# Performance work log

Hardware: AMD Instinct MI355X
Metric: run time of the kernel (lower is better)

The kernel has to match this reference:

```python
import jax, jax.numpy as jnp
import numpy as np

B, C, H, W = 2, 64, 128, 128
HEADS, DH = 8, 32
DN = ('NCHW', 'OIHW', 'NCHW')


def _conv(x, w, pad):
    return jax.lax.conv_general_dilated(x, w, (1, 1), [(pad, pad), (pad, pad)], dimension_numbers=DN)


def _rconv3(x, w):
    # Conv3x3 module: ReflectionPad2d(1) then 3x3 VALID conv, no bias
    xp = jnp.pad(x, ((0, 0), (0, 0), (1, 1), (1, 1)), mode='reflect')
    return jax.lax.conv_general_dilated(xp, w, (1, 1), 'VALID', dimension_numbers=DN)


def _prelu(x, a):
    return jnp.where(x > 0, x, a * x)


def _l2n(x):
    # F.normalize(p=2, dim=-1), eps=1e-12
    return x / jnp.maximum(jnp.linalg.norm(x, axis=-1, keepdims=True), 1e-12)


def _ln(y, g, b):
    mu = y.mean(-1, keepdims=True)
    v = ((y - mu) ** 2).mean(-1, keepdims=True)
    return (y - mu) / jnp.sqrt(v + 1e-5) * g + b


def _qco(x, w1, sw, sb, t1w, t1b, t2w, t2b):
    # QCO_C with level_num == C
    b, Cc = x.shape[0], x.shape[1]
    L = Cc
    x1 = _rconv3(x, w1)
    x_ave = _conv(jnp.mean(x1, (2, 3), keepdims=True), sw, 0) + sb[None, :, None, None]  # [b,C,1,1]
    xq = x_ave.reshape(b, Cc)
    mn = xq.min(-1, keepdims=True)
    mx = xq.max(-1, keepdims=True)
    qs = jnp.arange(L, dtype=x.dtype)
    ql = (2.0 * qs + 1.0) / (2.0 * L) * (mx - mn) + mn  # [b,L]
    inter = (ql[:, 1] - ql[:, 0])[:, None, None]  # [b,1,1]
    quant = 1.0 - jnp.abs(ql[:, None, :] - xq[:, :, None])  # [b,C,L]
    quant = quant * (quant > 1.0 - inter)
    sta = quant.sum(1)  # [b,L]
    sta = sta / sta.sum(-1, keepdims=True)
    out = jnp.concatenate([sta[:, :, None, None], x_ave], axis=1)  # [b,2C,1,1]
    out = jax.nn.relu(_conv(out, t1w, 0) + t1b[None, :, None, None])
    out = jax.nn.relu(_conv(out, t2w, 0) + t2b[None, :, None, None])
    return out  # [b,C,1,1]


def _attention(x, w_down, w_mid, w_up, wq_l, wk_m, wv_m, wq_h, rescale,
               w_proj_l, b_proj_l, w_proj_h, b_proj_h,
               qco_w1, qco_sca_w, qco_sca_b, qco_t1_w, qco_t1_b, qco_t2_w, qco_t2_b,
               rsp_w1, rsp_prelu, rsp_w2, c31_w1, c31_prelu, c31_w2, c31_w3):
    b, Cc, Hh, Ww = x.shape
    n = Hh * Ww
    # QKV conv projections (Conv2d, zero pad 1, no bias)
    xCL = jnp.moveaxis(_conv(x, w_down, 1), 1, -1)  # [b,h,w,C]
    xCM = jnp.moveaxis(_conv(x, w_mid, 1), 1, -1)   # [b,h,w,2C]
    xCH = jnp.moveaxis(_conv(x, w_up, 1), 1, -1)    # [b,h,w,3C]
    xL = xCL.reshape(b, n, Cc)
    xM = xCM.reshape(b, n, 2 * Cc)
    xH = xCH.reshape(b, n, 3 * Cc)

    def to_heads(t, d):  # [b,n,heads*d] -> [b,heads,d,n]
        return t.reshape(b, n, HEADS, d).transpose(0, 2, 3, 1)

    q_l = _l2n(to_heads(xL @ wq_l.T, DH))            # [b,heads,DH,n]
    k_m = _l2n(to_heads(xM @ wk_m.T, 2 * DH))        # [b,heads,2DH,n]
    v_m = to_heads(xM @ wv_m.T, 2 * DH)              # [b,heads,2DH,n]
    q_h = _l2n(to_heads(xH @ wq_h.T, 3 * DH))        # [b,heads,3DH,n]

    attn_l = jax.nn.softmax(jnp.einsum('bhdn,bhen->bhde', q_l, k_m) * rescale, axis=-1)  # [b,heads,DH,2DH]
    attn_h = jax.nn.softmax(jnp.einsum('bhdn,bhen->bhde', q_h, k_m) * rescale, axis=-1)  # [b,heads,3DH,2DH]

    x_l = jnp.einsum('bhde,bhen->bhdn', attn_l, v_m).transpose(0, 3, 1, 2).reshape(b, n, HEADS * DH)
    x_h = jnp.einsum('bhde,bhen->bhdn', attn_h, v_m).transpose(0, 3, 1, 2).reshape(b, n, HEADS * 3 * DH)
    # NOTE: torch code does .view(b, c, h, w) on [b, n, c] output -> raw memory reinterpretation,
    # which is exactly jnp.reshape here (faithful to the original, including this quirk).
    out_cl = (x_l @ w_proj_l.T + b_proj_l).reshape(b, Cc, Hh, Ww)
    out_ch = (x_h @ w_proj_h.T + b_proj_h).reshape(b, 3 * Cc, Hh, Ww)

    Hcat = jnp.concatenate([out_cl, out_ch], axis=1)  # [b,4C,h,w]
    H_out = _rconv3(_prelu(_rconv3(Hcat, rsp_w1), rsp_prelu), rsp_w2)  # ReshapeBlock -> [b,C,h,w]
    att_before = _qco(jnp.moveaxis(xCL, -1, 1), qco_w1, qco_sca_w, qco_sca_b,
                      qco_t1_w, qco_t1_b, qco_t2_w, qco_t2_b)  # [b,C,1,1]
    t = _prelu(_rconv3(H_out, c31_w1), c31_prelu)
    H_add = _conv(_rconv3(t, c31_w2), c31_w3, 0)  # Conv3_1
    return H_add + H_out * att_before


def _ff_block(z, g, bb, w1, b1, w2, b2):
    # PreNorm(LayerNorm over channel) + FeedForward(Linear, LeakyReLU(0.01), Linear)
    y = jnp.moveaxis(z, 1, -1)
    y = _ln(y, g, bb)
    y = y @ w1.T + b1
    y = jnp.where(y > 0, y, 0.01 * y)
    y = y @ w2.T + b2
    return jnp.moveaxis(y, -1, 1)


def _forward(x, w_down, w_mid, w_up, wq_l, wk_m, wv_m, wq_h, rescale,
             w_proj_l, b_proj_l, w_proj_h, b_proj_h,
             qco_w1, qco_sca_w, qco_sca_b, qco_t1_w, qco_t1_b, qco_t2_w, qco_t2_b,
             rsp_w1, rsp_prelu, rsp_w2, c31_w1, c31_prelu, c31_w2, c31_w3,
             ln1_g, ln1_b, ff1_w1, ff1_b1, ff1_w2, ff1_b2,
             ln2_g, ln2_b, ff2_w1, ff2_b1, ff2_w2, ff2_b2):
    out1 = _attention(x, w_down, w_mid, w_up, wq_l, wk_m, wv_m, wq_h, rescale,
                      w_proj_l, b_proj_l, w_proj_h, b_proj_h,
                      qco_w1, qco_sca_w, qco_sca_b, qco_t1_w, qco_t1_b, qco_t2_w, qco_t2_b,
                      rsp_w1, rsp_prelu, rsp_w2, c31_w1, c31_prelu, c31_w2, c31_w3) + x
    out2 = _ff_block(out1, ln1_g, ln1_b, ff1_w1, ff1_b1, ff1_w2, ff1_b2) + out1
    out3 = _ff_block(out2, ln2_g, ln2_b, ff2_w1, ff2_b1, ff2_w2, ff2_b2) + out1
    return out3


def setup_inputs() -> dict:
    keys = iter(jax.random.split(jax.random.key(0), 48))

    def rn(shape, s=0.05):
        return (jax.random.normal(next(keys), shape, jnp.float32) * s)

    d = {
        'x': rn((B, C, H, W), 1.0),
        'w_down': rn((C, C, 3, 3)), 'w_mid': rn((2 * C, C, 3, 3)), 'w_up': rn((3 * C, C, 3, 3)),
        'wq_l': rn((HEADS * DH, C)), 'wk_m': rn((2 * HEADS * DH, 2 * C)),
        'wv_m': rn((2 * HEADS * DH, 2 * C)), 'wq_h': rn((3 * HEADS * DH, 3 * C)),
        'rescale': jnp.ones((HEADS, 1, 1), jnp.float32),
        'w_proj_l': rn((C, HEADS * DH)), 'b_proj_l': rn((C,)),
        'w_proj_h': rn((3 * C, 3 * HEADS * DH)), 'b_proj_h': rn((3 * C,)),
        'qco_w1': rn((C, C, 3, 3)), 'qco_sca_w': rn((C, C, 1, 1)), 'qco_sca_b': rn((C,)),
        'qco_t1_w': rn((C, 2 * C, 1, 1)), 'qco_t1_b': rn((C,)),
        'qco_t2_w': rn((C, C, 1, 1)), 'qco_t2_b': rn((C,)),
        'rsp_w1': rn((C, 4 * C, 3, 3)), 'rsp_prelu': jnp.array(0.25, jnp.float32), 'rsp_w2': rn((C, C, 3, 3)),
        'c31_w1': rn((C, C, 3, 3)), 'c31_prelu': jnp.array(0.25, jnp.float32),
        'c31_w2': rn((C, C, 3, 3)), 'c31_w3': rn((C, C, 1, 1)),
        'ln1_g': jnp.ones((C,), jnp.float32), 'ln1_b': jnp.zeros((C,), jnp.float32),
        'ff1_w1': rn((C, C)), 'ff1_b1': rn((C,)), 'ff1_w2': rn((C, C)), 'ff1_b2': rn((C,)),
        'ln2_g': jnp.ones((C,), jnp.float32), 'ln2_b': jnp.zeros((C,), jnp.float32),
        'ff2_w1': rn((C, C)), 'ff2_b1': rn((C,)), 'ff2_w2': rn((C, C)), 'ff2_b2': rn((C,)),
    }
    return d


def reference(x, w_down, w_mid, w_up, wq_l, wk_m, wv_m, wq_h, rescale,
              w_proj_l, b_proj_l, w_proj_h, b_proj_h,
              qco_w1, qco_sca_w, qco_sca_b, qco_t1_w, qco_t1_b, qco_t2_w, qco_t2_b,
              rsp_w1, rsp_prelu, rsp_w2, c31_w1, c31_prelu, c31_w2, c31_w3,
              ln1_g, ln1_b, ff1_w1, ff1_b1, ff1_w2, ff1_b2,
              ln2_g, ln2_b, ff2_w1, ff2_b1, ff2_w2, ff2_b2):
    return _forward(x, w_down, w_mid, w_up, wq_l, wk_m, wv_m, wq_h, rescale,
                    w_proj_l, b_proj_l, w_proj_h, b_proj_h,
                    qco_w1, qco_sca_w, qco_sca_b, qco_t1_w, qco_t1_b, qco_t2_w, qco_t2_b,
                    rsp_w1, rsp_prelu, rsp_w2, c31_w1, c31_prelu, c31_w2, c31_w3,
                    ln1_g, ln1_b, ff1_w1, ff1_b1, ff1_w2, ff1_b2,
                    ln2_g, ln2_b, ff2_w1, ff2_b1, ff2_w2, ff2_b2)
```

## Files before the change

### kernel.cpp

```cpp
#include <hip/hip_runtime.h>
#include <hip/hip_bf16.h>
#include <stdint.h>

typedef __hip_bfloat16 bf16;
typedef __attribute__((ext_vector_type(8))) __bf16 bf8v;
typedef __attribute__((ext_vector_type(8))) short short8;
typedef __attribute__((ext_vector_type(4))) short short4v;
typedef __attribute__((ext_vector_type(4))) float f32x4;
#define DEVINL __device__ __forceinline__
#define MFMA16(a,b,c) __builtin_amdgcn_mfma_f32_16x16x32_bf16((a),(b),(c),0,0,0)

DEVINL short f2bs(float f) { bf16 h = __float2bfloat16(f); return *reinterpret_cast<short*>(&h); }
DEVINL float bs2f(short s) { bf16 h = *reinterpret_cast<bf16*>(&s); return __bfloat162float(h); }


static const size_t OFF_ZBF   = 0;
static const size_t OFF_WTQ   = 29360128;
static const size_t OFF_WTR1  = 29802496;
static const size_t OFF_WTR2  = 30097408;
static const size_t OFF_WTC1  = 30171136;
static const size_t OFF_WTF   = 30244864;
static const size_t OFF_W1T   = 30318592;
static const size_t OFF_SCAWT = 30466048;
static const size_t OFF_T1WT  = 30482432;
static const size_t OFF_T2WT  = 30515200;
static const size_t OFF_GB    = 31645696;
static const size_t OFF_WQLB  = 32235520;
static const size_t OFF_WKMB  = 32268288;
static const size_t OFF_WQHB  = 32399360;
static const size_t OFF_T1    = 41082880;
static const size_t OFF_UL    = 41345024;
static const size_t OFF_UK    = 41476096;
static const size_t OFF_T1H   = 42000384;
static const size_t OFF_UH    = 42786816;
static const size_t OFF_NORMS = 43966464;
static const size_t OFF_ATTL  = 43978752;
static const size_t OFF_ATTH  = 44109824;
static const size_t OFF_WEL   = 44503040;
static const size_t OFF_WEH   = 44765184;
static const size_t OFF_ACATB = 45813760;
static const size_t OFF_TSUM  = 45944832;
static const size_t OFF_ATTB  = 45949440;
static const size_t OFF_HCATB = 45949952;
static const size_t OFF_MIDB  = 62727168;
static const size_t OFF_HOUTB = 66921472;
static const size_t OFF_WFFB  = 71115776;
static const size_t OFF_GPART = 79504384;
static const size_t OFF_HCATT = 79504384;
static const size_t OFF_XT    = 98378752;
static const size_t WS_BYTES  = 102573056;

__global__ __launch_bounds__(256) void k_prep_all(
    const float* __restrict__ wd, const float* __restrict__ wm,
    const float* __restrict__ wu, const float* __restrict__ rw1,
    const float* __restrict__ rw2, const float* __restrict__ cw1,
    const float* __restrict__ wql, const float* __restrict__ wkm,
    const float* __restrict__ wqh,
    const float* __restrict__ c31w3, const float* __restrict__ c31w2,
    const float* __restrict__ qw1, const float* __restrict__ qscaw,
    const float* __restrict__ qt1w, const float* __restrict__ qt2w,
    const float* __restrict__ f11, const float* __restrict__ f12,
    const float* __restrict__ f21, const float* __restrict__ f22,
    const float* __restrict__ x,
    bf16* __restrict__ wtq, bf16* __restrict__ wtr1,
    bf16* __restrict__ wtr2, bf16* __restrict__ wtc1,
    bf16* __restrict__ wqlb, bf16* __restrict__ wkmb,
    bf16* __restrict__ wqhb, bf16* __restrict__ wtf,
    float* __restrict__ w1t, float* __restrict__ scawt,
    float* __restrict__ t1wt, float* __restrict__ t2wt,
    bf16* __restrict__ wffb, short* __restrict__ xt) {
  __shared__ short sT[64][72];
  const int t = threadIdx.x;
  if (blockIdx.x >= 3040) {
    const int j = blockIdx.x - 3040;
    const int b = j >> 8, p0 = (j & 255) * 64;
    for (int i = t; i < 1024; i += 256) {
      int c = i >> 4, p4 = (i & 15) * 4;
      float4 g = *(const float4*)&x[(((size_t)(b * 64 + c)) << 14) + p0 + p4];
      sT[p4 + 0][c] = f2bs(g.x);
      sT[p4 + 1][c] = f2bs(g.y);
      sT[p4 + 2][c] = f2bs(g.z);
      sT[p4 + 3][c] = f2bs(g.w);
    }
    __syncthreads();
    for (int i = t; i < 512; i += 256) {
      int p = i >> 3, co = (i & 7) * 8;
      *(short8*)&xt[((((size_t)b << 14) + p0 + p)) * 64 + co] = *(short8*)&sT[p][co];
    }
    return;
  }
  int i = blockIdx.x * 256 + t;
  if (i < 221184) {
    int tap = i / 24576, r = i % 24576, oc = r >> 6, ic = r & 63;
    float v;
    if (oc < 64)       v = wd[(oc * 64 + ic) * 9 + tap];
    else if (oc < 192) v = wm[((oc - 64) * 64 + ic) * 9 + tap];
    else               v = wu[((oc - 192) * 64 + ic) * 9 + tap];
    wtq[i] = __float2bfloat16(v);
  } else if (i < 368640) {
    int j = i - 221184;
    int tap = j / 16384, r = j % 16384, oc = r >> 8, ic = r & 255;
    wtr1[j] = __float2bfloat16(rw1[(oc * 256 + ic) * 9 + tap]);
  } else if (i < 405504) {
    int j = i - 368640;
    int tap = j / 4096, r = j % 4096, oc = r >> 6, ic = r & 63;
    wtr2[j] = __float2bfloat16(rw2[(oc * 64 + ic) * 9 + tap]);
  } else if (i < 442368) {
    int j = i - 405504;
    int tap = j / 4096, r = j % 4096, oc = r >> 6, ic = r & 63;
    wtc1[j] = __float2bfloat16(cw1[(oc * 64 + ic) * 9 + tap]);
  } else if (i < 458752) {
    int j = i - 442368; wqlb[j] = __float2bfloat16(wql[j]);
  } else if (i < 524288) {
    int j = i - 458752; wkmb[j] = __float2bfloat16(wkm[j]);
  } else if (i < 671744) {
    int j = i - 524288; wqhb[j] = __float2bfloat16(wqh[j]);
  } else if (i < 708608) {
    int j = i - 671744;
    int tap = j / 4096, r = j % 4096, o = r >> 6, ic = r & 63;
    float s = 0.f;
    for (int m = 0; m < 64; m++)
      s = fmaf(c31w3[o * 64 + m], c31w2[(m * 64 + ic) * 9 + tap], s);
    wtf[j] = __float2bfloat16(s);
  } else if (i < 745472) {
    int o = i - 708608;
    int c = o & 63, rest = o >> 6, jj = rest / 9, tap = rest % 9;
    w1t[o] = qw1[(c * 64 + jj) * 9 + tap];
  } else if (i < 749568) {
    int o = i - 745472;
    int c = o & 63, jj = o >> 6;
    scawt[o] = qscaw[c * 64 + jj];
  } else if (i < 757760) {
    int o = i - 749568;
    int c = o & 63, jj = o >> 6;
    t1wt[o] = qt1w[c * 128 + jj];
  } else if (i < 761856) {
    int o = i - 757760;
    int c = o & 63, jj = o >> 6;
    t2wt[o] = qt2w[c * 64 + jj];
  } else if (i < 778240) {
    int j = i - 761856;
    int stage = j >> 12, r = j & 4095;
    const float* src = (stage == 0) ? f11 : (stage == 1) ? f12 : (stage == 2) ? f21 : f22;
    wffb[j] = __float2bfloat16(src[r]);
  }
}

__global__ __launch_bounds__(256) void k_transph(const short* __restrict__ hc,
                                                 short* __restrict__ ht) {
  __shared__ short sT[64][72];
  const int t = threadIdx.x, b = blockIdx.z, p0 = blockIdx.x * 64, c0 = blockIdx.y * 64;
  for (int i = t; i < 512; i += 256) {
    int c = i >> 3, qo = (i & 7) * 8;
    short8 v = *(const short8*)&hc[(((size_t)(b * 256 + c0 + c)) << 14) + p0 + qo];
#pragma unroll
    for (int u = 0; u < 8; u++) sT[qo + u][c] = v[u];
  }
  __syncthreads();
  for (int i = t; i < 512; i += 256) {
    int q = i >> 3, co = (i & 7) * 8;
    *(short8*)&ht[((size_t)(b * 16384 + p0 + q)) * 256 + c0 + co] = *(short8*)&sT[q][co];
  }
}

__global__ __launch_bounds__(256) void k_convq(
    const short* __restrict__ xt, const short* __restrict__ wtq,
    bf16* __restrict__ zbf)
{
  __shared__ short sX[3][130][72];
  const int t = threadIdx.x, lane = t & 63, wv = t >> 6;
  const int y = blockIdx.x, ocg = blockIdx.y, b = blockIdx.z;

  for (int i = t; i < 3120; i += 256) {
    int ko = i & 7, c2 = i >> 3, col = c2 % 130, row = c2 / 130;
    int gy = y + row - 1, gx = col - 1;
    short8 vv;
    if ((gy >= 0) & (gy < 128) & (gx >= 0) & (gx < 128)) {
      vv = *(const short8*)&xt[((size_t)b * 1048576 + (size_t)((gy << 7) + gx) * 64) + ko * 8];
    } else {
#pragma unroll
      for (int u = 0; u < 8; u++) vv[u] = 0;
    }
    *(short8*)&sX[row][col][ko * 8] = vv;
  }
  __syncthreads();

  const f32x4 zero = {0.f, 0.f, 0.f, 0.f};
  f32x4 acc[3][8];
#pragma unroll
  for (int m = 0; m < 3; m++)
// ... 113 lines not shown
  __shared__ float sv[64][68];
  __shared__ short sy[64][72];
  __shared__ float spar[8][64];
  const int t = threadIdx.x, lane = t & 63, wv = t >> 6;
  const int y = blockIdx.x, x0 = blockIdx.y * 64, b = blockIdx.z;

  if (t < 64) {
    spar[0][t] = g1[t]; spar[1][t] = be1[t]; spar[2][t] = b11[t]; spar[3][t] = b12[t];
    spar[4][t] = g2[t]; spar[5][t] = be2[t]; spar[6][t] = b21[t]; spar[7][t] = b22[t];
  }
  for (int i = t; i < 1584; i += 256) {
    int ko = i & 7, c2 = i >> 3, col = c2 % 66, row = c2 / 66;
    int gy = y + row - 1, gx = x0 + col - 1;
    gy = gy < 0 ? 1 : (gy > 127 ? 126 : gy);
    gx = gx < 0 ? 1 : (gx > 127 ? 126 : gx);
    *(short8*)&sX[row][col][ko * 8] =
        *(const short8*)&in[(size_t)b * 1048576 + (size_t)((gy << 7) + gx) * 64 + ko * 8];
  }
  __syncthreads();

  const f32x4 zero = {0.f, 0.f, 0.f, 0.f};
  {
    f32x4 cacc[4] = {zero, zero, zero, zero};
#pragma unroll
    for (int tap = 0; tap < 9; tap++) {
      const int ky = tap / 3, kx = tap % 3;
#pragma unroll
      for (int kk = 0; kk < 2; kk++) {
        const int kb = kk * 32 + (lane >> 4) * 8;
        bf8v afr = *(const bf8v*)&Wt[(size_t)(tap * 64 + wv * 16 + (lane & 15)) * 64 + kb];
#pragma unroll
        for (int n = 0; n < 4; n++) {
          bf8v bfr = *(const bf8v*)&sX[ky][n * 16 + (lane & 15) + kx][kb];
          cacc[n] = MFMA16(afr, bfr, cacc[n]);
        }
      }
    }
    const int oc0 = wv * 16 + ((lane >> 4) << 2);
    float4 av = *(const float4*)&attb[b * 64 + oc0];
#pragma unroll
    for (int n = 0; n < 4; n++) {
      const int pxl = n * 16 + (lane & 15);
      const int gpx = (y << 7) + x0 + pxl;
      short4v hv = *(const short4v*)&houtpm[((size_t)(b * 16384 + gpx)) * 64 + oc0];
#pragma unroll
      for (int r = 0; r < 4; r++)
        sv[pxl][oc0 + r] = cacc[n][r] + bs2f(hv[r]) * (&av.x)[r] +
                           x_nchw[(((size_t)(b * 64 + oc0 + r)) << 14) + gpx];
    }
  }
  __syncthreads();

  const int chq = ((lane >> 4) << 2);
  const int pxl = wv * 16 + (lane & 15);
  float4 vv[4];
#pragma unroll
  for (int m = 0; m < 4; m++) vv[m] = *(const float4*)&sv[pxl][m * 16 + chq];

  f32x4 facc[4];

#define LN_F(SRCV, GI, BI)                                                      \
  {                                                                             \
    float s1 = 0.f, s2 = 0.f;                                                   \
    _Pragma("unroll")                                                           \
    for (int m = 0; m < 4; m++)                                                 \
      _Pragma("unroll")                                                         \
      for (int r = 0; r < 4; r++) {                                             \
        float vx = (&SRCV[m].x)[r];                                             \
        s1 += vx; s2 += vx * vx;                                                \
      }                                                                         \
    s1 += __shfl_xor(s1, 16); s1 += __shfl_xor(s1, 32);                         \
    s2 += __shfl_xor(s2, 16); s2 += __shfl_xor(s2, 32);                         \
    float mu = s1 * (1.f / 64.f);                                               \
    float var = fmaxf(s2 * (1.f / 64.f) - mu * mu, 0.f);                        \
    float rstd = 1.f / sqrtf(var + 1e-5f);                                      \
    _Pragma("unroll")                                                           \
    for (int m = 0; m < 4; m++) {                                               \
      short4v ss;                                                               \
      _Pragma("unroll")                                                         \
      for (int r = 0; r < 4; r++) {                                             \
        int ch = m * 16 + chq + r;                                              \
        ss[r] = f2bs(((&SRCV[m].x)[r] - mu) * rstd * spar[GI][ch] + spar[BI][ch]); \
      }                                                                         \
      *(short4v*)&sy[pxl][m * 16 + chq] = ss;                                   \
    }                                                                           \
  }

#define MM_F(SIDX)                                                              \
  {                                                                             \
    _Pragma("unroll")                                                           \
    for (int m = 0; m < 4; m++) facc[m] = zero;                                 \
    _Pragma("unroll")                                                           \
    for (int kk = 0; kk < 2; kk++) {                                            \
      const int kb = kk * 32 + (lane >> 4) * 8;                                 \
      bf8v bfr = *(const bf8v*)&sy[wv * 16 + (lane & 15)][kb];                  \
      _Pragma("unroll")                                                         \
      for (int m = 0; m < 4; m++) {                                             \
        bf8v afr = *(const bf8v*)&wffb[(size_t)(SIDX) * 4096 +                  \
                                       (m * 16 + (lane & 15)) * 64 + kb];       \
        facc[m] = MFMA16(afr, bfr, facc[m]);                                    \
      }                                                                         \
    }                                                                           \
  }

  LN_F(vv, 0, 1);
  MM_F(0);
#pragma unroll
  for (int m = 0; m < 4; m++) {
    short4v ss;
#pragma unroll
    for (int r = 0; r < 4; r++) {
      float h = facc[m][r] + spar[2][m * 16 + chq + r];
      h = h > 0.f ? h : 0.01f * h;
      ss[r] = f2bs(h);
    }
    *(short4v*)&sy[pxl][m * 16 + chq] = ss;
  }
  MM_F(1);
  float4 o2v[4];
#pragma unroll
  for (int m = 0; m < 4; m++)
#pragma unroll
    for (int r = 0; r < 4; r++)
      (&o2v[m].x)[r] = facc[m][r] + spar[3][m * 16 + chq + r] + (&vv[m].x)[r];
  LN_F(o2v, 4, 5);
  MM_F(2);
#pragma unroll
  for (int m = 0; m < 4; m++) {
    short4v ss;
#pragma unroll
    for (int r = 0; r < 4; r++) {
      float h = facc[m][r] + spar[6][m * 16 + chq + r];
      h = h > 0.f ? h : 0.01f * h;
      ss[r] = f2bs(h);
    }
    *(short4v*)&sy[pxl][m * 16 + chq] = ss;
  }
  MM_F(3);
  const int gpx = (y << 7) + x0 + pxl;
#pragma unroll
  for (int m = 0; m < 4; m++)
#pragma unroll
    for (int r = 0; r < 4; r++) {
      const int ch = m * 16 + chq + r;
      outp[(((size_t)(b * 64 + ch)) << 14) + gpx] =
          facc[m][r] + spar[7][ch] + (&vv[m].x)[r];
    }
#undef LN_F
#undef MM_F
}

__global__ __launch_bounds__(256) void k_gramm(const short* __restrict__ Z,
                                               float* __restrict__ Gp) {
  int rem = blockIdx.x, ti = 0;
  while (rem >= 6 - ti) { rem -= 6 - ti; ti++; }
  const int tj = ti + rem;
  const int kc = blockIdx.y, b = blockIdx.z;
  __shared__ short sA[64][72];
  __shared__ short sB[64][72];
  const int t = threadIdx.x, lane = t & 63, wv = t >> 6;
  const int wo = wv & 1, wp = wv >> 1;
  const f32x4 zero = {0.f, 0.f, 0.f, 0.f};
  f32x4 acc[2][2];
#pragma unroll
  for (int m = 0; m < 2; m++)
#pragma unroll
    for (int n = 0; n < 2; n++) acc[m][n] = zero;
  const size_t zb = (size_t)b * 6291456;
  const int k0 = kc * 1024;
  for (int ks = 0; ks < 1024; ks += 64) {
    __syncthreads();
    for (int i = t; i < 512; i += 256) {
      int r = i >> 3, ko = i & 7;
      *(short8*)&sA[r][ko * 8] =
          *(const short8*)&Z[zb + ((size_t)(ti * 64 + r) << 14) + k0 + ks + ko * 8];
      *(short8*)&sB[r][ko * 8] =
          *(const short8*)&Z[zb + ((size_t)(tj * 64 + r) << 14) + k0 + ks + ko * 8];
    }
    __syncthreads();
#pragma unroll
    for (int kk = 0; kk < 2; kk++) {
      const int kb = kk * 32 + (lane >> 4) * 8;
      bf8v bfr[2];
#pragma unroll
      for (int n = 0; n < 2; n++)
        bfr[n] = *(const bf8v*)&sB[wp * 32 + n * 16 + (lane & 15)][kb];
#pragma unroll
      for (int m = 0; m < 2; m++) {
        bf8v afr = *(const bf8v*)&sA[wo * 32 + m * 16 + (lane & 15)][kb];
#pragma unroll
        for (int n = 0; n < 2; n++)
          acc[m][n] = MFMA16(afr, bfr[n], acc[m][n]);
      }
    }
  }
  float* gp = Gp + ((size_t)(kc * 2 + b)) * 147456;
#pragma unroll
  for (int m = 0; m < 2; m++)
#pragma unroll
    for (int n = 0; n < 2; n++)
#pragma unroll
      for (int r = 0; r < 4; r++) {
        const int row = ti * 64 + wo * 32 + m * 16 + ((lane >> 4) << 2) + r;
        const int col = tj * 64 + wp * 32 + n * 16 + (lane & 15);
        float v = acc[m][n][r];
        gp[(size_t)row * 384 + col] = v;
        if (ti != tj) gp[(size_t)col * 384 + row] = v;
      }
}

__global__ __launch_bounds__(256) void k_gt(const float* __restrict__ Gp,
                                            bf16* __restrict__ Gb,
                                            const bf16* __restrict__ Z,
                                            float* __restrict__ Tsum) {
  __shared__ float sc[16];
  __shared__ float red[4][9];
  const int t = threadIdx.x;
  if (blockIdx.x < 1152) {
    int i = blockIdx.x * 256 + t;
    if (i >= 294912) return;
    int b = i / 147456, e = i % 147456;
    float s = 0.f;
#pragma unroll
    for (int c = 0; c < 16; c++) s += Gp[(size_t)(c * 2 + b) * 147456 + e];
    Gb[(size_t)b * 147456 + e] = __float2bfloat16(s);
    return;
  }
  const int bid = blockIdx.x - 1152;
  const int c = bid & 63, b = bid >> 6;
  const bf16* src = Z + (((size_t)(b * 384 + c)) << 14);
  float a9[9] = {};
  for (int i = t; i < 2048; i += 256) {
    int y = i >> 4, x0 = (i & 15) * 8;
    short8 v8 = *(const short8*)&src[(y << 7) + x0];
    float vs[8], s8 = 0.f;
#pragma unroll
    for (int u = 0; u < 8; u++) { vs[u] = bs2f(v8[u]); s8 += vs[u]; }
    a9[0] += s8;
    int ri = (y == 0) ? 0 : (y == 1) ? 1 : (y == 126) ? 2 : (y == 127) ? 3 : -1;
    if (ri >= 0) a9[1 + ri] += s8;
    if (x0 == 0)   { a9[5] += vs[0]; a9[6] += vs[1]; }
    if (x0 == 120) { a9[7] += vs[6]; a9[8] += vs[7]; }
    if (ri >= 0) {
      if (x0 == 0)   { sc[ri * 4 + 0] = vs[0]; sc[ri * 4 + 1] = vs[1]; }
      if (x0 == 120) { sc[ri * 4 + 2] = vs[6]; sc[ri * 4 + 3] = vs[7]; }
    }
  }
#pragma unroll
  for (int q = 0; q < 9; q++)
#pragma unroll
    for (int o = 32; o; o >>= 1) a9[q] += __shfl_xor(a9[q], o);
  const int w = t >> 6;
  if ((t & 63) == 0)
#pragma unroll
    for (int q = 0; q < 9; q++) red[w][q] = a9[q];
  __syncthreads();
  if (t == 0) {
    float s9[9];
#pragma unroll
    for (int q = 0; q < 9; q++) s9[q] = red[0][q] + red[1][q] + red[2][q] + red[3][q];
    const float T = s9[0];
    float R[4] = {s9[1], s9[2], s9[3], s9[4]};
    const float C0 = s9[5], C1 = s9[6], C126 = s9[7], C127 = s9[8];
    float rs[4][3];
#pragma unroll
    for (int ri = 0; ri < 4; ri++) {
      rs[ri][0] = R[ri] - sc[ri * 4 + 3] + sc[ri * 4 + 1];
      rs[ri][1] = R[ri];
      rs[ri][2] = R[ri] - sc[ri * 4 + 0] + sc[ri * 4 + 2];
    }
    float A3[3] = {T - C127 + C1, T, T - C0 + C126};
#pragma unroll
    for (int dx = 0; dx < 3; dx++) {
      Tsum[bid * 9 + 0 * 3 + dx] = A3[dx] - rs[3][dx] + rs[1][dx];
      Tsum[bid * 9 + 1 * 3 + dx] = A3[dx];
      Tsum[bid * 9 + 2 * 3 + dx] = A3[dx] - rs[0][dx] + rs[2][dx];
    }
  }
}

struct MJobs5 {
  const short* A[5];
  float* C[5];
  int lda[5], K[5], r0[5], c0[5], ldc[5];
  long sC[5];
  int nx[5], b0[6];
};

__global__ __launch_bounds__(256) void k_mgemm5(MJobs5 J, const short* __restrict__ Gb) {
  const int bx = blockIdx.x, z = blockIdx.y;
  int j = 0;
  while (bx >= J.b0[j + 1]) j++;
  const int local = bx - J.b0[j];
  const int xn = local % J.nx[j], ym = local / J.nx[j];
  const int t = threadIdx.x, lane = t & 63, wv = t >> 6;
  const short* Gp = Gb + (size_t)z * 147456;
  const short* Ap = J.A[j];
  const int K = J.K[j], lda = J.lda[j];
  const int m0 = ym * 64 + wv * 16, n0 = xn * 64;
  const int gc0 = J.c0[j] + n0, r0 = J.r0[j];
  const f32x4 zero = {0.f, 0.f, 0.f, 0.f};
  f32x4 acc[4] = {zero, zero, zero, zero};
  for (int kk = 0; kk < K; kk += 32) {
    const int kb = kk + (lane >> 4) * 8;
    bf8v afr = *(const bf8v*)&Ap[(size_t)(m0 + (lane & 15)) * lda + kb];
#pragma unroll
    for (int n = 0; n < 4; n++) {
      bf8v bfr = *(const bf8v*)&Gp[(size_t)(gc0 + n * 16 + (lane & 15)) * 384 + r0 + kb];
      acc[n] = MFMA16(afr, bfr, acc[n]);
    }
  }
  float* Cp = J.C[j] + (size_t)z * J.sC[j];
  const int mq = m0 + ((lane >> 4) << 2);
#pragma unroll
  for (int n = 0; n < 4; n++) {
    const int nc = n0 + n * 16 + (lane & 15);
#pragma unroll
    for (int r = 0; r < 4; r++)
      Cp[(size_t)(mq + r) * J.ldc[j] + nc] = acc[n][r];
  }
}

__global__ __launch_bounds__(256) void k_pixm(
    const short* __restrict__ Z, const short* __restrict__ Acatb,
    const float* __restrict__ bl, const float* __restrict__ bh,
    bf16* __restrict__ hcat)
{
  const int p0 = blockIdx.x * 64, ocg = blockIdx.y, b = blockIdx.z;
  __shared__ short sA[64][136];
  __shared__ short sB[64][136];
  const int t = threadIdx.x, lane = t & 63, wv = t >> 6;
  for (int i = t; i < 1024; i += 256) {
    int oc = i >> 4, ko = i & 15;
    *(short8*)&sA[oc][ko * 8] =
        *(const short8*)&Acatb[((size_t)(b * 256 + ocg * 64 + oc)) * 128 + ko * 8];
  }
  for (int i = t; i < 1024; i += 256) {
    int px = i & 63, ko = i >> 6;
    short8 vv;
#pragma unroll
    for (int u = 0; u < 8; u++)
      vv[u] = Z[((size_t)(b * 384 + 64 + ko * 8 + u) << 14) + p0 + px];
    *(short8*)&sB[px][ko * 8] = vv;
  }
  __syncthreads();
  const f32x4 zero = {0.f, 0.f, 0.f, 0.f};
  f32x4 acc[4] = {zero, zero, zero, zero};
#pragma unroll
  for (int kk = 0; kk < 4; kk++) {
    const int kb = kk * 32 + (lane >> 4) * 8;
    bf8v afr = *(const bf8v*)&sA[wv * 16 + (lane & 15)][kb];
#pragma unroll
    for (int n = 0; n < 4; n++) {
      bf8v bfr = *(const bf8v*)&sB[n * 16 + (lane & 15)][kb];
      acc[n] = MFMA16(afr, bfr, acc[n]);
    }
  }
  const size_t hbase = (size_t)b * 4194304;
#pragma unroll
  for (int n = 0; n < 4; n++) {
    const int px = p0 + n * 16 + (lane & 15);
#pragma unroll
    for (int r = 0; r < 4; r++) {
      const int oc = ocg * 64 + wv * 16 + ((lane >> 4) << 2) + r;
      float v = acc[n][r] + (oc < 64 ? bl[oc] : bh[oc - 64]);
      size_t addr = (oc < 64) ? hbase + (size_t)px * 64 + oc
                              : hbase + 1048576 + (size_t)px * 192 + (oc - 64);
      hcat[addr] = __float2bfloat16(v);
    }
  }
}

struct Jobs2 {
  const float* A[2]; const float* B[2];
  int K[2]; int lda[2];
  long sB[2];
  int nx[2]; int b0[3]; int co[2];
};

__global__ __launch_bounds__(256) void k_sgemm2b(Jobs2 J, bf16* __restrict__ Cb) {
  __shared__ float sa[16][17];
  __shared__ float sb[16][17];
  const int bx = blockIdx.x, z = blockIdx.y;
  int j = (bx >= J.b0[1]) ? 1 : 0;
  const int local = bx - J.b0[j];
  const int x = local % J.nx[j], y = local / J.nx[j];
  const int tx = threadIdx.x & 15, ty = threadIdx.x >> 4;
  const float* Ap = J.A[j];
  const float* Bp = J.B[j] + (size_t)z * J.sB[j];
  const int K = J.K[j], lda = J.lda[j];
  const int m = y * 16 + ty, n = x * 16 + tx;
  float acc = 0.f;
  for (int k0 = 0; k0 < K; k0 += 16) {
    sa[ty][tx] = Ap[(size_t)m * lda + k0 + tx];
    sb[ty][tx] = Bp[(size_t)(k0 + ty) * 128 + n];
    __syncthreads();
#pragma unroll
    for (int kk = 0; kk < 16; kk++) acc = fmaf(sa[ty][kk], sb[kk][tx], acc);
    __syncthreads();
  }
  Cb[(size_t)z * 32768 + J.co[j] + (size_t)m * 128 + n] = __float2bfloat16(acc);
}

__global__ __launch_bounds__(256) void k_nq(
    const float* __restrict__ UL, const float* __restrict__ UK,
    const float* __restrict__ UH,
    const float* __restrict__ wql, const float* __restrict__ wkm,
    const float* __restrict__ wqh, float* __restrict__ norms,
    const float* __restrict__ Tsum, const float* __restrict__ w1t,
    const float* __restrict__ scawt, const float* __restrict__ scab,
    const float* __restrict__ t1wt, const float* __restrict__ t1b,
    const float* __restrict__ t2wt, const float* __restrict__ t2b,
    float* __restrict__ attb)
{
  __shared__ float sm[64], sxq[64], scat[128], sh1[64];
  const int t = threadIdx.x, lane = t & 63;
  if (blockIdx.x < 768) {
    const int row = blockIdx.x * 4 + (t >> 6);
    const int b = row >= 1536 ? 1 : 0;
    const int r = row - b * 1536;
    const float* u; const float* wv; int K;
    if (r < 256)      { K = 64;  u = UL + (size_t)(b * 256 + r) * 64;          wv = wql + (size_t)r * 64; }
    else if (r < 768) { int e = r - 256; K = 128; u = UK + (size_t)(b * 512 + e) * 128; wv = wkm + (size_t)e * 128; }
    else              { int d = r - 768; K = 192; u = UH + (size_t)(b * 768 + d) * 192; wv = wqh + (size_t)d * 192; }
    float s = 0.f;
    for (int k = lane; k < K; k += 64) s = fmaf(u[k], wv[k], s);
#pragma unroll
    for (int o = 32; o; o >>= 1) s += __shfl_xor(s, o);
    if (lane == 0) norms[b * 1536 + r] = fmaxf(sqrtf(fmaxf(s, 0.f)), 1e-12f);
    return;
  }
  const int b = blockIdx.x - 768, c = t;
  if (t < 64) {
    float acc = 0.f;
    for (int j = 0; j < 64; j++) {
#pragma unroll
      for (int tap = 0; tap < 9; tap++)
        acc = fmaf(w1t[((j * 9 + tap) << 6) + c], Tsum[(b * 64 + j) * 9 + tap], acc);
    }
    sm[c] = acc * (1.f / 16384.f);
  }
  __syncthreads();
  if (t < 64) {
    float xa = scab[c];
    for (int j = 0; j < 64; j++) xa = fmaf(scawt[(j << 6) + c], sm[j], xa);
    sxq[c] = xa;
  }
  __syncthreads();
  if (t < 64) {
    float xa = sxq[c];
    float mn = xa, mx = xa;
#pragma unroll
    for (int o = 32; o; o >>= 1) {
      mn = fminf(mn, __shfl_xor(mn, o));
      mx = fmaxf(mx, __shfl_xor(mx, o));
    }
    float inter = (mx - mn) * (1.f / 64.f);
    float ql = (2.f * c + 1.f) / 128.f * (mx - mn) + mn;
    float sta = 0.f;
    for (int j = 0; j < 64; j++) {
      float q = 1.f - fabsf(ql - sxq[j]);
      sta += (q > 1.f - inter) ? q : 0.f;
    }
    float tot = sta;
#pragma unroll
    for (int o = 32; o; o >>= 1) tot += __shfl_xor(tot, o);
    sta = sta / fmaxf(tot, 1e-30f);
    scat[c] = sta; scat[64 + c] = xa;
  }
  __syncthreads();
  if (t < 64) {
    float h = t1b[c];
    for (int j = 0; j < 128; j++) h = fmaf(t1wt[(j << 6) + c], scat[j], h);
    h = fmaxf(h, 0.f);
    sh1[c] = h;
  }
  __syncthreads();
  if (t < 64) {
    float o2 = t2b[c];
    for (int j = 0; j < 64; j++) o2 = fmaf(t2wt[(j << 6) + c], sh1[j], o2);
    attb[b * 64 + c] = fmaxf(o2, 0.f);
  }
}

__global__ __launch_bounds__(256) void k_attn(
    const float* __restrict__ T1, const float* __restrict__ T1H,
    const float* __restrict__ wkm, const float* __restrict__ norms,
    const float* __restrict__ rescale,
    float* __restrict__ attL, float* __restrict__ attH)
{
  const int h = blockIdx.x, cy = blockIdx.y, b = blockIdx.z;
  const int t = threadIdx.x;
  __shared__ float sK[64 * 129];
  __shared__ float sQ[32 * 129];
  __shared__ float sNk[64];
  const int isL = (cy == 0);
  const int rbase = isL ? 0 : (cy - 1) * 32;
  const float* TQ = isL ? (T1 + (size_t)(b * 256 + h * 32) * 128)
                        : (T1H + (size_t)(b * 768 + h * 96 + rbase) * 128);
  for (int idx = t; idx < 8192; idx += 256) {
    int e = idx >> 7, k = idx & 127;
    sK[e * 129 + k] = wkm[(size_t)(h * 64 + e) * 128 + k];
  }
  for (int idx = t; idx < 4096; idx += 256) {
    int r = idx >> 7, k = idx & 127;
    sQ[r * 129 + k] = TQ[(size_t)r * 128 + k];
  }
  if (t < 64) sNk[t] = norms[b * 1536 + 256 + h * 64 + t];
  __syncthreads();

  const int w = t >> 6, lane = t & 63;
  const float rs = rescale[h];
  for (int r = w; r < 32; r += 4) {
    float s = 0.f;
    for (int k = 0; k < 128; k++) s = fmaf(sQ[r * 129 + k], sK[lane * 129 + k], s);
    float nq = norms[b * 1536 + (isL ? (h * 32 + r) : (768 + h * 96 + rbase + r))];
    float logit = s / (nq * sNk[lane]) * rs;
    float m = logit;
#pragma unroll
    for (int o = 32; o; o >>= 1) m = fmaxf(m, __shfl_xor(m, o));
    float p = __expf(logit - m);
    float den = p;
#pragma unroll
    for (int o = 32; o; o >>= 1) den += __shfl_xor(den, o);
    float av = p / den;
    if (isL) attL[((size_t)(b * 8 + h) * 32 + r) * 64 + lane] = av;
    else     attH[((size_t)(b * 8 + h) * 96 + rbase + r) * 64 + lane] = av;
  }
}

__global__ __launch_bounds__(256) void k_weff(
    const float* __restrict__ attL, const float* __restrict__ attH,
    const float* __restrict__ wvm,
    float* __restrict__ WeL, float* __restrict__ WeH)
{
  const int h = blockIdx.x, br = blockIdx.y, b = blockIdx.z;
  const int M = br ? 96 : 32;
  __shared__ float sAt[96 * 64];
  __shared__ float sV[64 * 132];
  const int t = threadIdx.x;
  const float* asrc = br ? attH + (size_t)(b * 8 + h) * 96 * 64
                         : attL + (size_t)(b * 8 + h) * 32 * 64;
  for (int idx = t; idx < M * 64; idx += 256) sAt[idx] = asrc[idx];
  for (int idx = t; idx < 8192; idx += 256) {
    int e = idx >> 7, k = idx & 127;
    sV[e * 132 + k] = wvm[(size_t)(h * 64 + e) * 128 + k];
  }
  __syncthreads();
  const int jg = t & 31, rw = t >> 5;
  float* dst = br ? WeH + (size_t)(b * 768 + h * 96) * 128
                  : WeL + (size_t)(b * 256 + h * 32) * 128;
  for (int r = rw; r < M; r += 8) {
    float4 acc = make_float4(0.f, 0.f, 0.f, 0.f);
    for (int e = 0; e < 64; e++) {
      float a = sAt[r * 64 + e];
      float4 v4 = *(const float4*)&sV[e * 132 + jg * 4];
      acc.x = fmaf(a, v4.x, acc.x);
      acc.y = fmaf(a, v4.y, acc.y);
      acc.z = fmaf(a, v4.z, acc.z);
      acc.w = fmaf(a, v4.w, acc.w);
    }
    *(float4*)&dst[(size_t)r * 128 + jg * 4] = acc;
  }
}

extern "C" void kernel_launch(void* const* d_in, const int* in_sizes, int n_in,
                              void* d_out, int out_size, void* d_ws, size_t ws_size,
                              hipStream_t stream)
{
  if (ws_size < WS_BYTES) return;
  char* ws = (char*)d_ws;

  const float* x       = (const float*)d_in[0];
  const float* w_down  = (const float*)d_in[1];
  const float* w_mid   = (const float*)d_in[2];
  const float* w_up    = (const float*)d_in[3];
  const float* wq_l    = (const float*)d_in[4];
  const float* wk_m    = (const float*)d_in[5];
  const float* wv_m    = (const float*)d_in[6];
  const float* wq_h    = (const float*)d_in[7];
  const float* rescale = (const float*)d_in[8];
  const float* w_proj_l= (const float*)d_in[9];
  const float* b_proj_l= (const float*)d_in[10];
  const float* w_proj_h= (const float*)d_in[11];
  const float* b_proj_h= (const float*)d_in[12];
  const float* qco_w1  = (const float*)d_in[13];
  const float* qsca_w  = (const float*)d_in[14];
  const float* qsca_b  = (const float*)d_in[15];
  const float* qt1_w   = (const float*)d_in[16];
  const float* qt1_b   = (const float*)d_in[17];
  const float* qt2_w   = (const float*)d_in[18];
  const float* qt2_b   = (const float*)d_in[19];
  const float* rsp_w1  = (const float*)d_in[20];
  const float* rsp_pr  = (const float*)d_in[21];
  const float* rsp_w2  = (const float*)d_in[22];
  const float* c31_w1  = (const float*)d_in[23];
  const float* c31_pr  = (const float*)d_in[24];
  const float* c31_w2  = (const float*)d_in[25];
  const float* c31_w3  = (const float*)d_in[26];
  const float* ln1_g   = (const float*)d_in[27];
  const float* ln1_b   = (const float*)d_in[28];
  const float* ff1_w1  = (const float*)d_in[29];
  const float* ff1_b1  = (const float*)d_in[30];
  const float* ff1_w2  = (const float*)d_in[31];
  const float* ff1_b2  = (const float*)d_in[32];
  const float* ln2_g   = (const float*)d_in[33];
  const float* ln2_b   = (const float*)d_in[34];
  const float* ff2_w1  = (const float*)d_in[35];
  const float* ff2_b1  = (const float*)d_in[36];
  const float* ff2_w2  = (const float*)d_in[37];
  const float* ff2_b2  = (const float*)d_in[38];

  bf16*  zbf   = (bf16*)(ws + OFF_ZBF);
  bf16*  wtq   = (bf16*)(ws + OFF_WTQ);
  bf16*  wtr1  = (bf16*)(ws + OFF_WTR1);
  bf16*  wtr2  = (bf16*)(ws + OFF_WTR2);
  bf16*  wtc1  = (bf16*)(ws + OFF_WTC1);
  bf16*  wtf   = (bf16*)(ws + OFF_WTF);
  float* w1t   = (float*)(ws + OFF_W1T);
  float* scawt = (float*)(ws + OFF_SCAWT);
  float* t1wt  = (float*)(ws + OFF_T1WT);
  float* t2wt  = (float*)(ws + OFF_T2WT);
  bf16*  Gb    = (bf16*)(ws + OFF_GB);
  bf16*  wqlb  = (bf16*)(ws + OFF_WQLB);
  bf16*  wkmb  = (bf16*)(ws + OFF_WKMB);
  bf16*  wqhb  = (bf16*)(ws + OFF_WQHB);
  float* gpart = (float*)(ws + OFF_GPART);
  float* T1    = (float*)(ws + OFF_T1);
  float* UL    = (float*)(ws + OFF_UL);
  float* UK    = (float*)(ws + OFF_UK);
  float* T1H   = (float*)(ws + OFF_T1H);
  float* UH    = (float*)(ws + OFF_UH);
  float* norms = (float*)(ws + OFF_NORMS);
  float* attL  = (float*)(ws + OFF_ATTL);
  float* attH  = (float*)(ws + OFF_ATTH);
  float* WeL   = (float*)(ws + OFF_WEL);
  float* WeH   = (float*)(ws + OFF_WEH);
  bf16*  acatb = (bf16*)(ws + OFF_ACATB);
  float* tsum  = (float*)(ws + OFF_TSUM);
  float* attb  = (float*)(ws + OFF_ATTB);
  bf16*  hcatb = (bf16*)(ws + OFF_HCATB);
  short* hcatT = (short*)(ws + OFF_HCATT);
  short* midb  = (short*)(ws + OFF_MIDB);
  short* houtb = (short*)(ws + OFF_HOUTB);
  bf16*  wffb  = (bf16*)(ws + OFF_WFFB);
  short* xt    = (short*)(ws + OFF_XT);

  k_prep_all<<<dim3(3552), 256, 0, stream>>>(
      w_down, w_mid, w_up, rsp_w1, rsp_w2, c31_w1, wq_l, wk_m, wq_h,
      c31_w3, c31_w2, qco_w1, qsca_w, qt1_w, qt2_w,
      ff1_w1, ff1_w2, ff2_w1, ff2_w2, x,
      wtq, wtr1, wtr2, wtc1, wqlb, wkmb, wqhb, wtf,
      w1t, scawt, t1wt, t2wt, wffb, xt);

  k_convq<<<dim3(128, 2, 2), 256, 0, stream>>>(xt, (const short*)wtq, zbf);

  k_gramm<<<dim3(21, 16, 2), 256, 0, stream>>>((const short*)zbf, gpart);

  k_gt<<<dim3(1280), 256, 0, stream>>>(gpart, Gb, zbf, tsum);

  MJobs5 M5;
  M5.A[0] = (const short*)wqlb; M5.lda[0] = 64;  M5.K[0] = 64;  M5.r0[0] = 0;   M5.c0[0] = 64;  M5.C[0] = T1;  M5.ldc[0] = 128; M5.sC[0] = 32768;  M5.nx[0] = 2;
  M5.A[1] = (const short*)wqlb; M5.lda[1] = 64;  M5.K[1] = 64;  M5.r0[1] = 0;   M5.c0[1] = 0;   M5.C[1] = UL;  M5.ldc[1] = 64;  M5.sC[1] = 16384;  M5.nx[1] = 1;
  M5.A[2] = (const short*)wkmb; M5.lda[2] = 128; M5.K[2] = 128; M5.r0[2] = 64;  M5.c0[2] = 64;  M5.C[2] = UK;  M5.ldc[2] = 128; M5.sC[2] = 65536;  M5.nx[2] = 2;
  M5.A[3] = (const short*)wqhb; M5.lda[3] = 192; M5.K[3] = 192; M5.r0[3] = 192; M5.c0[3] = 64;  M5.C[3] = T1H; M5.ldc[3] = 128; M5.sC[3] = 98304;  M5.nx[3] = 2;
  M5.A[4] = (const short*)wqhb; M5.lda[4] = 192; M5.K[4] = 192; M5.r0[4] = 192; M5.c0[4] = 192; M5.C[4] = UH;  M5.ldc[4] = 192; M5.sC[4] = 147456; M5.nx[4] = 3;
  M5.b0[0] = 0; M5.b0[1] = 8; M5.b0[2] = 12; M5.b0[3] = 28; M5.b0[4] = 52; M5.b0[5] = 88;
  k_mgemm5<<<dim3(88, 2), 256, 0, stream>>>(M5, (const short*)Gb);

  k_nq<<<dim3(770), 256, 0, stream>>>(UL, UK, UH, wq_l, wk_m, wq_h, norms,
                                      tsum, w1t, scawt, qsca_b, t1wt, qt1_b, t2wt, qt2_b, attb);

  k_attn<<<dim3(8, 4, 2), 256, 0, stream>>>(T1, T1H, wk_m, norms, rescale, attL, attH);
  k_weff<<<dim3(8, 2, 2), 256, 0, stream>>>(attL, attH, wv_m, WeL, WeH);

  Jobs2 J2;
  J2.A[0] = w_proj_l; J2.B[0] = WeL; J2.K[0] = 256; J2.lda[0] = 256; J2.sB[0] = 32768; J2.nx[0] = 8; J2.co[0] = 0;
  J2.A[1] = w_proj_h; J2.B[1] = WeH; J2.K[1] = 768; J2.lda[1] = 768; J2.sB[1] = 98304; J2.nx[1] = 8; J2.co[1] = 8192;
  J2.b0[0] = 0; J2.b0[1] = 32; J2.b0[2] = 128;
  k_sgemm2b<<<dim3(128, 2), 256, 0, stream>>>(J2, acatb);

  k_pixm<<<dim3(256, 4, 2), 256, 0, stream>>>((const short*)zbf, (const short*)acatb,
                                              b_proj_l, b_proj_h, hcatb);

  k_transph<<<dim3(256, 4, 2), 256, 0, stream>>>((const short*)hcatb, hcatT);

  k_conv64<1><<<dim3(128, 2, 2), 256, 0, stream>>>(
      hcatT, 256, 4194304L, 256, (const short*)wtr1, midb, rsp_pr);
  k_conv64<0><<<dim3(128, 2, 2), 256, 0, stream>>>(
      midb, 64, 1048576L, 64, (const short*)wtr2, houtb, nullptr);

  k_conv64<1><<<dim3(128, 2, 2), 256, 0, stream>>>(
      houtb, 64, 1048576L, 64, (const short*)wtc1, midb, c31_pr);

  k_convff<<<dim3(128, 2, 2), 256, 0, stream>>>(
      midb, (const short*)wtf, houtb, attb, x, (const short*)wffb,
      ln1_g, ln1_b, ff1_b1, ff1_b2, ln2_g, ln2_b, ff2_b1, ff2_b2,
      (float*)d_out);
}
```

Measured before the change: 263.1 us.

## Fuse norm, attention softmax and value-weight kernels into one launch

Merges the norm computation, the attention softmax and the effective-weight product into a single kernel, with one extra block per batch running the QCO branch. This drops two launches and the global round trips for norms and attention matrices. Each block now computes its own key and query norms serially from shared memory, which adds redundant work and uses more shared memory per block. Separately, the Gram kernel drops three blocks in its tile-pair grid and replaces the index loop with lookup tables.

```diff
diff --git a/kernel.cpp b/kernel.cpp
--- a/kernel.cpp
+++ b/kernel.cpp
@@ -33,9 +33,6 @@
 static const size_t OFF_UK    = 41476096;
 static const size_t OFF_T1H   = 42000384;
 static const size_t OFF_UH    = 42786816;
-static const size_t OFF_NORMS = 43966464;
-static const size_t OFF_ATTL  = 43978752;
-static const size_t OFF_ATTH  = 44109824;
 static const size_t OFF_WEL   = 44503040;
 static const size_t OFF_WEH   = 44765184;
 static const size_t OFF_ACATB = 45813760;
@@ -455,9 +452,9 @@
 
 __global__ __launch_bounds__(256) void k_gramm(const short* __restrict__ Z,
                                                float* __restrict__ Gp) {
-  int rem = blockIdx.x, ti = 0;
-  while (rem >= 6 - ti) { rem -= 6 - ti; ti++; }
-  const int tj = ti + rem;
+  static const char TIa[18] = {0,0,0,1,1,2,1,1,1,2,2,2,3,3,3,4,4,5};
+  static const char TJa[18] = {0,1,2,1,2,2,3,4,5,3,4,5,3,4,5,4,5,5};
+  const int ti = TIa[blockIdx.x], tj = TJa[blockIdx.x];
   const int kc = blockIdx.y, b = blockIdx.z;
   __shared__ short sA[64][72];
   __shared__ short sB[64][72];
@@ -705,98 +702,85 @@
   Cb[(size_t)z * 32768 + J.co[j] + (size_t)m * 128 + n] = __float2bfloat16(acc);
 }
 
-__global__ __launch_bounds__(256) void k_nq(
+__global__ __launch_bounds__(256) void k_attnw(
+    const float* __restrict__ T1, const float* __restrict__ T1H,
     const float* __restrict__ UL, const float* __restrict__ UK,
     const float* __restrict__ UH,
     const float* __restrict__ wql, const float* __restrict__ wkm,
-    const float* __restrict__ wqh, float* __restrict__ norms,
+    const float* __restrict__ wqh, const float* __restrict__ wvm,
+    const float* __restrict__ rescale,
+    float* __restrict__ WeL, float* __restrict__ WeH,
     const float* __restrict__ Tsum, const float* __restrict__ w1t,
     const float* __restrict__ scawt, const float* __restrict__ scab,
     const float* __restrict__ t1wt, const float* __restrict__ t1b,
     const float* __restrict__ t2wt, const float* __restrict__ t2b,
     float* __restrict__ attb)
 {
+  __shared__ float sK[64 * 129];
+  __shared__ float sV[64 * 132];
+  __shared__ float sQ[32 * 129];
+  __shared__ float sAt[32 * 64];
+  __shared__ float sNk[64];
+  __shared__ float sNq[32];
   __shared__ float sm[64], sxq[64], scat[128], sh1[64];
-  const int t = threadIdx.x, lane = t & 63;
-  if (blockIdx.x < 768) {
-    const int row = blockIdx.x * 4 + (t >> 6);
-    const int b = row >= 1536 ? 1 : 0;
-    const int r = row - b * 1536;
-    const float* u; const float* wv; int K;
-    if (r < 256)      { K = 64;  u = UL + (size_t)(b * 256 + r) * 64;          wv = wql + (size_t)r * 64; }
-    else if (r < 768) { int e = r - 256; K = 128; u = UK + (size_t)(b * 512 + e) * 128; wv = wkm + (size_t)e * 128; }
-    else              { int d = r - 768; K = 192; u = UH + (size_t)(b * 768 + d) * 192; wv = wqh + (size_t)d * 192; }
-    float s = 0.f;
-    for (int k = lane; k < K; k += 64) s = fmaf(u[k], wv[k], s);
-#pragma unroll
-    for (int o = 32; o; o >>= 1) s += __shfl_xor(s, o);
-    if (lane == 0) norms[b * 1536 + r] = fmaxf(sqrtf(fmaxf(s, 0.f)), 1e-12f);
+  const int t = threadIdx.x, b = blockIdx.y;
+
+  if (blockIdx.x == 32) {
+    const int c = t;
+    if (t < 64) {
+      float acc = 0.f;
+      for (int j = 0; j < 64; j++) {
+#pragma unroll
+        for (int tap = 0; tap < 9; tap++)
+          acc = fmaf(w1t[((j * 9 + tap) << 6) + c], Tsum[(b * 64 + j) * 9 + tap], acc);
+      }
+      sm[c] = acc * (1.f / 16384.f);
+    }
+    __syncthreads();
+    if (t < 64) {
+      float xa = scab[c];
+      for (int j = 0; j < 64; j++) xa = fmaf(scawt[(j << 6) + c], sm[j], xa);
+      sxq[c] = xa;
+    }
+    __syncthreads();
+    if (t < 64) {
+      float xa = sxq[c];
+      float mn = xa, mx = xa;
+#pragma unroll
+      for (int o = 32; o; o >>= 1) {
+        mn = fminf(mn, __shfl_xor(mn, o));
+        mx = fmaxf(mx, __shfl_xor(mx, o));
+      }
+      float inter = (mx - mn) * (1.f / 64.f);
+      float ql = (2.f * c + 1.f) / 128.f * (mx - mn) + mn;
+      float sta = 0.f;
+      for (int j = 0; j < 64; j++) {
+        float q = 1.f - fabsf(ql - sxq[j]);
+        sta += (q > 1.f - inter) ? q : 0.f;
+      }
+      float tot = sta;
+#pragma unroll
+      for (int o = 32; o; o >>= 1) tot += __shfl_xor(tot, o);
+      sta = sta / fmaxf(tot, 1e-30f);
+      scat[c] = sta; scat[64 + c] = xa;
+    }
+    __syncthreads();
+    if (t < 64) {
+      float h = t1b[c];
+      for (int j = 0; j < 128; j++) h = fmaf(t1wt[(j << 6) + c], scat[j], h);
+      h = fmaxf(h, 0.f);
+      sh1[c] = h;
+    }
+    __syncthreads();
+    if (t < 64) {
+      float o2 = t2b[c];
+      for (int j = 0; j < 64; j++) o2 = fmaf(t2wt[(j << 6) + c], sh1[j], o2);
+      attb[b * 64 + c] = fmaxf(o2, 0.f);
+    }
     return;
   }
-  const int b = blockIdx.x - 768, c = t;
-  if (t < 64) {
-    float acc = 0.f;
-    for (int j = 0; j < 64; j++) {
-#pragma unroll
-      for (int tap = 0; tap < 9; tap++)
-        acc = fmaf(w1t[((j * 9 + tap) << 6) + c], Tsum[(b * 64 + j) * 9 + tap], acc);
-    }
-    sm[c] = acc * (1.f / 16384.f);
-  }
-  __syncthreads();
-  if (t < 64) {
-    float xa = scab[c];
-    for (int j = 0; j < 64; j++) xa = fmaf(scawt[(j << 6) + c], sm[j], xa);
-    sxq[c] = xa;
-  }
-  __syncthreads();
-  if (t < 64) {
-    float xa = sxq[c];
-    float mn = xa, mx = xa;
-#pragma unroll
-    for (int o = 32; o; o >>= 1) {
-      mn = fminf(mn, __shfl_xor(mn, o));
-      mx = fmaxf(mx, __shfl_xor(mx, o));
-    }
-    float inter = (mx - mn) * (1.f / 64.f);
-    float ql = (2.f * c + 1.f) / 128.f * (mx - mn) + mn;
-    float sta = 0.f;
-    for (int j = 0; j < 64; j++) {
-      float q = 1.f - fabsf(ql - sxq[j]);
-      sta += (q > 1.f - inter) ? q : 0.f;
-    }
-    float tot = sta;
-#pragma unroll
-    for (int o = 32; o; o >>= 1) tot += __shfl_xor(tot, o);
-    sta = sta / fmaxf(tot, 1e-30f);
-    scat[c] = sta; scat[64 + c] = xa;
-  }
-  __syncthreads();
-  if (t < 64) {
-    float h = t1b[c];
-    for (int j = 0; j < 128; j++) h = fmaf(t1wt[(j << 6) + c], scat[j], h);
-    h = fmaxf(h, 0.f);
-    sh1[c] = h;
-  }
-  __syncthreads();
-  if (t < 64) {
-    float o2 = t2b[c];
-    for (int j = 0; j < 64; j++) o2 = fmaf(t2wt[(j << 6) + c], sh1[j], o2);
-    attb[b * 64 + c] = fmaxf(o2, 0.f);
-  }
-}
-
-__global__ __launch_bounds__(256) void k_attn(
-    const float* __restrict__ T1, const float* __restrict__ T1H,
-    const float* __restrict__ wkm, const float* __restrict__ norms,
-    const float* __restrict__ rescale,
-    float* __restrict__ attL, float* __restrict__ attH)
-{
-  const int h = blockIdx.x, cy = blockIdx.y, b = blockIdx.z;
-  const int t = threadIdx.x;
-  __shared__ float sK[64 * 129];
-  __shared__ float sQ[32 * 129];
-  __shared__ float sNk[64];
+
+  const int h = blockIdx.x >> 2, cy = blockIdx.x & 3;
   const int isL = (cy == 0);
   const int rbase = isL ? 0 : (cy - 1) * 32;
   const float* TQ = isL ? (T1 + (size_t)(b * 256 + h * 32) * 128)
@@ -804,12 +788,30 @@
   for (int idx = t; idx < 8192; idx += 256) {
     int e = idx >> 7, k = idx & 127;
     sK[e * 129 + k] = wkm[(size_t)(h * 64 + e) * 128 + k];
+    sV[e * 132 + k] = wvm[(size_t)(h * 64 + e) * 128 + k];
   }
   for (int idx = t; idx < 4096; idx += 256) {
     int r = idx >> 7, k = idx & 127;
     sQ[r * 129 + k] = TQ[(size_t)r * 128 + k];
   }
-  if (t < 64) sNk[t] = norms[b * 1536 + 256 + h * 64 + t];
+  __syncthreads();
+
+  if (t < 64) {
+    const float* u = UK + (size_t)(b * 512 + h * 64 + t) * 128;
+    float s = 0.f;
+    for (int k = 0; k < 128; k++) s = fmaf(u[k], sK[t * 129 + k], s);
+    sNk[t] = fmaxf(sqrtf(fmaxf(s, 0.f)), 1e-12f);
+  } else if (t >= 128 && t < 160) {
+    const int r = t - 128;
+    const float* u; const float* wv; int K;
+    if (isL) { K = 64;  u = UL + (size_t)(b * 256 + h * 32 + r) * 64;
+               wv = wql + (size_t)(h * 32 + r) * 64; }
+    else     { K = 192; u = UH + (size_t)(b * 768 + h * 96 + rbase + r) * 192;
+               wv = wqh + (size_t)(h * 96 + rbase + r) * 192; }
+    float s = 0.f;
+    for (int k = 0; k < K; k++) s = fmaf(u[k], wv[k], s);
+    sNq[r] = fmaxf(sqrtf(fmaxf(s, 0.f)), 1e-12f);
+  }
   __syncthreads();
 
   const int w = t >> 6, lane = t & 63;
@@ -817,8 +819,7 @@
   for (int r = w; r < 32; r += 4) {
     float s = 0.f;
     for (int k = 0; k < 128; k++) s = fmaf(sQ[r * 129 + k], sK[lane * 129 + k], s);
-    float nq = norms[b * 1536 + (isL ? (h * 32 + r) : (768 + h * 96 + rbase + r))];
-    float logit = s / (nq * sNk[lane]) * rs;
+    float logit = s / (sNq[r] * sNk[lane]) * rs;
     float m = logit;
 #pragma unroll
     for (int o = 32; o; o >>= 1) m = fmaxf(m, __shfl_xor(m, o));
@@ -826,34 +827,14 @@
     float den = p;
 #pragma unroll
     for (int o = 32; o; o >>= 1) den += __shfl_xor(den, o);
-    float av = p / den;
-    if (isL) attL[((size_t)(b * 8 + h) * 32 + r) * 64 + lane] = av;
-    else     attH[((size_t)(b * 8 + h) * 96 + rbase + r) * 64 + lane] = av;
-  }
-}
-
-__global__ __launch_bounds__(256) void k_weff(
-    const float* __restrict__ attL, const float* __restrict__ attH,
-    const float* __restrict__ wvm,
-    float* __restrict__ WeL, float* __restrict__ WeH)
-{
-  const int h = blockIdx.x, br = blockIdx.y, b = blockIdx.z;
-  const int M = br ? 96 : 32;
-  __shared__ float sAt[96 * 64];
-  __shared__ float sV[64 * 132];
-  const int t = threadIdx.x;
-  const float* asrc = br ? attH + (size_t)(b * 8 + h) * 96 * 64
-                         : attL + (size_t)(b * 8 + h) * 32 * 64;
-  for (int idx = t; idx < M * 64; idx += 256) sAt[idx] = asrc[idx];
-  for (int idx = t; idx < 8192; idx += 256) {
-    int e = idx >> 7, k = idx & 127;
-    sV[e * 132 + k] = wvm[(size_t)(h * 64 + e) * 128 + k];
-  }
-  __syncthreads();
+    sAt[r * 64 + lane] = p / den;
+  }
+  __syncthreads();
+
   const int jg = t & 31, rw = t >> 5;
-  float* dst = br ? WeH + (size_t)(b * 768 + h * 96) * 128
-                  : WeL + (size_t)(b * 256 + h * 32) * 128;
-  for (int r = rw; r < M; r += 8) {
+  float* dst = isL ? (WeL + (size_t)(b * 256 + h * 32) * 128)
+                   : (WeH + (size_t)(b * 768 + h * 96 + rbase) * 128);
+  for (int r = rw; r < 32; r += 8) {
     float4 acc = make_float4(0.f, 0.f, 0.f, 0.f);
     for (int e = 0; e < 64; e++) {
       float a = sAt[r * 64 + e];
@@ -934,9 +915,6 @@
   float* UK    = (float*)(ws + OFF_UK);
   float* T1H   = (float*)(ws + OFF_T1H);
   float* UH    = (float*)(ws + OFF_UH);
-  float* norms = (float*)(ws + OFF_NORMS);
-  float* attL  = (float*)(ws + OFF_ATTL);
-  float* attH  = (float*)(ws + OFF_ATTH);
   float* WeL   = (float*)(ws + OFF_WEL);
   float* WeH   = (float*)(ws + OFF_WEH);
   bf16*  acatb = (bf16*)(ws + OFF_ACATB);
@@ -958,7 +936,7 @@
 
   k_convq<<<dim3(128, 2, 2), 256, 0, stream>>>(xt, (const short*)wtq, zbf);
 
-  k_gramm<<<dim3(21, 16, 2), 256, 0, stream>>>((const short*)zbf, gpart);
+  k_gramm<<<dim3(18, 16, 2), 256, 0, stream>>>((const short*)zbf, gpart);
 
   k_gt<<<dim3(1280), 256, 0, stream>>>(gpart, Gb, zbf, tsum);
 
@@ -971,11 +949,9 @@
   M5.b0[0] = 0; M5.b0[1] = 8; M5.b0[2] = 12; M5.b0[3] = 28; M5.b0[4] = 52; M5.b0[5] = 88;
   k_mgemm5<<<dim3(88, 2), 256, 0, stream>>>(M5, (const short*)Gb);
 
-  k_nq<<<dim3(770), 256, 0, stream>>>(UL, UK, UH, wq_l, wk_m, wq_h, norms,
-                                      tsum, w1t, scawt, qsca_b, t1wt, qt1_b, t2wt, qt2_b, attb);
-
-  k_attn<<<dim3(8, 4, 2), 256, 0, stream>>>(T1, T1H, wk_m, norms, rescale, attL, attH);
-  k_weff<<<dim3(8, 2, 2), 256, 0, stream>>>(attL, attH, wv_m, WeL, WeH);
+  k_attnw<<<dim3(33, 2), 256, 0, stream>>>(
+      T1, T1H, UL, UK, UH, wq_l, wk_m, wq_h, wv_m, rescale, WeL, WeH,
+      tsum, w1t, scawt, qsca_b, t1wt, qt1_b, t2wt, qt2_b, attb);
 
   Jobs2 J2;
   J2.A[0] = w_proj_l; J2.B[0] = WeL; J2.K[0] = 256; J2.lda[0] = 256; J2.sB[0] = 32768; J2.nx[0] = 8; J2.co[0] = 0;
```

Result: faster. 243.7 us (-7.4%).
